# Kernel optimization log

Hardware: AMD Instinct MI355X
Metric: run time of the kernel (lower is better)

Reference implementation:

```python
import jax, jax.numpy as jnp
import numpy as np

N = 100000   # particles
D = 100      # grid cells per dimension


def setup_inputs() -> dict:
    rng = np.random.default_rng(0)
    d = 0.05  # cell_size in source
    # distinct cells (module assumes one particle per cell)
    cells = rng.choice(D ** 3, size=N, replace=False)
    cz = cells // (D * D)
    cy = (cells // D) % D
    cx = cells % D
    jit = rng.uniform(-0.3, 0.3, size=(3, N)) * d  # |jitter| < 0.5*d keeps round(pos/d)==cell
    x = cx * d + jit[0]
    y = cy * d + jit[1]
    z = cz * d + jit[2]
    v = rng.standard_normal((3, N)) * 0.1
    kn = 60000.0
    restitution = 0.5
    alpha = -np.log(restitution) / np.pi
    gamma = alpha / np.sqrt(alpha ** 2 + 1.0)
    rho_p = 2700.0
    particle_mass = 4.0 / 3.0 * 3.1415 * d ** 3 * rho_p
    eta = 2.0 * gamma * np.sqrt(kn * particle_mass / 2.0)
    return {
        "compressed_x_grid": jnp.asarray(x, jnp.float32),
        "compressed_y_grid": jnp.asarray(y, jnp.float32),
        "compressed_z_grid": jnp.asarray(z, jnp.float32),
        "compressed_vx_grid": jnp.asarray(v[0], jnp.float32),
        "compressed_vy_grid": jnp.asarray(v[1], jnp.float32),
        "compressed_vz_grid": jnp.asarray(v[2], jnp.float32),
        "d": float(d),
        "kn": float(kn),
        "damping_coefficient_Eta": float(eta),
        "friction_coefficient": 0.5,
        "dt": 0.001,
        "input_shape": D,
        "filter_size": 5,
    }


def _forces(x, y, z, vx, vy, vz, d, kn, eta, grid_dim, filter_size):
    n = x.shape[0]
    eps = 1e-4
    # cell indices exactly as in the torch code: round(pos/d)
    cx = jnp.round(x / d).astype(jnp.int32)
    cy = jnp.round(y / d).astype(jnp.int32)
    cz = jnp.round(z / d).astype(jnp.int32)
    # dense particle-index grid; -1 = empty (replaces mask + particle_number_tensor)
    idx = -jnp.ones((grid_dim, grid_dim, grid_dim), jnp.int32)
    idx = idx.at[cz, cy, cx].set(jnp.arange(n, dtype=jnp.int32))
    # all filter_size^3 roll offsets; torch.roll wraps, so use modular indexing
    r = filter_size // 2
    ar = jnp.arange(-r, r + 1)
    off = jnp.stack(jnp.meshgrid(ar, ar, ar, indexing="ij"), axis=-1).reshape(-1, 3)  # [K,3] (sz,sy,sx)
    # pair (A at cell c) with (B at cell c - s): mask_contact_A==2 <=> occ[c] & occ[c-s]
    nz = (cz[:, None] - off[None, :, 0]) % grid_dim  # [N,K]
    ny = (cy[:, None] - off[None, :, 1]) % grid_dim
    nx = (cx[:, None] - off[None, :, 2]) % grid_dim
    B = idx[nz, ny, nx]                                   # [N,K] neighbor particle id or -1
    me = jnp.arange(n, dtype=jnp.int32)[:, None]
    valid = (B >= 0) & (B != me)                          # filters empty cells and self pairs (A != B)
    Bs = jnp.where(valid, B, 0)
    dxp = x[:, None] - x[Bs]
    dyp = y[:, None] - y[Bs]
    dzp = z[:, None] - z[Bs]
    dvx = vx[:, None] - vx[Bs]
    dvy = vy[:, None] - vy[Bs]
    dvz = vz[:, None] - vz[Bs]
    dist = jnp.sqrt(dxp * dxp + dyp * dyp + dzp * dzp)
    denom = jnp.maximum(eps, dist)
    contact = valid & (dist < 2.0 * d)
    # spring (collision) force on A, aggregated over neighbors (row-sum == scatter_add to A)
    coef = jnp.where(contact, kn * (dist - 2.0 * d) / denom, 0.0)
    fx_c = (coef * dxp).sum(axis=1)
    fy_c = (coef * dyp).sum(axis=1)
    fz_c = (coef * dzp).sum(axis=1)
    # normal damping force
    vn = (dvx * dxp + dvy * dyp + dvz * dzp) / denom
    dcoef = jnp.where(contact, eta * vn / denom, 0.0)
    fx_d = (dcoef * dxp).sum(axis=1)
    fy_d = (dcoef * dyp).sum(axis=1)
    fz_d = (dcoef * dzp).sum(axis=1)
    return jnp.stack([fx_c, fy_c, fz_c, fx_d, fy_d, fz_d])  # [6, N]


def reference(compressed_x_grid, compressed_y_grid, compressed_z_grid, compressed_vx_grid, compressed_vy_grid, compressed_vz_grid, d, kn, damping_coefficient_Eta, friction_coefficient, dt, input_shape, filter_size):
    return _forces(compressed_x_grid, compressed_y_grid, compressed_z_grid,
                   compressed_vx_grid, compressed_vy_grid, compressed_vz_grid,
                   d, kn, damping_coefficient_Eta, input_shape, filter_size)
```

## Files before the change

### kernel.cpp

```cpp
#include <hip/hip_runtime.h>

static const int DG = 100;
static const int PGD = DG + 4;
static const int PPLANE = PGD * PGD;
static const int PCELLS = PGD * PGD * PGD;


__global__ __launch_bounds__(256) void scatter_kernel(
    const float* __restrict__ x, const float* __restrict__ y, const float* __restrict__ z,
    const float* __restrict__ dptr, int* __restrict__ cell_idx, int n)
{
    int i = blockIdx.x * blockDim.x + threadIdx.x;
    if (i >= n) return;
    float inv_d = 1.0f / dptr[0];
    int cx = (int)roundf(x[i] * inv_d);
    int cy = (int)roundf(y[i] * inv_d);
    int cz = (int)roundf(z[i] * inv_d);
    cell_idx[((cz + 2) * PGD + (cy + 2)) * PGD + (cx + 2)] = i;
}

__global__ __launch_bounds__(256) void force_kernel(
    const float* __restrict__ x, const float* __restrict__ y, const float* __restrict__ z,
    const float* __restrict__ vx, const float* __restrict__ vy, const float* __restrict__ vz,
    const float* __restrict__ dptr, const float* __restrict__ knptr,
    const float* __restrict__ etaptr,
    const int* __restrict__ cell_idx, float* __restrict__ out, int n)
{
    int wid  = blockIdx.x * (blockDim.x >> 6) + (threadIdx.x >> 6);
    if (wid >= n) return;
    int lane = threadIdx.x & 63;
    int p = __builtin_amdgcn_readfirstlane(wid);

    float d    = dptr[0];
    float kn   = knptr[0];
    float eta  = etaptr[0];
    float inv_d = 1.0f / d;
    float two_d = 2.0f * d;

    float px = x[p], py = y[p], pz = z[p];
    float pvx = vx[p], pvy = vy[p], pvz = vz[p];
    int cx = (int)roundf(px * inv_d);
    int cy = (int)roundf(py * inv_d);
    int cz = (int)roundf(pz * inv_d);
    int base = ((cz + 2) * PGD + (cy + 2)) * PGD + (cx + 2);
    base = __builtin_amdgcn_readfirstlane(base);
    const int* __restrict__ g = cell_idx + base;

    int k1 = lane;
    int sz = k1 / 25; int r = k1 - sz * 25; int sy = r / 5; int sx = r - sy * 5;
    int off1 = (sz - 2) * PPLANE + (sy - 2) * PGD + (sx - 2);
    int k2 = lane + 64;
    bool has2 = (k2 < 125);
    int off2 = 0;
    if (has2) {
        sz = k2 / 25; r = k2 - sz * 25; sy = r / 5; sx = r - sy * 5;
        off2 = (sz - 2) * PPLANE + (sy - 2) * PGD + (sx - 2);
    }

    int B1 = g[off1];
    int B2 = has2 ? g[off2] : -1;

    float fxc = 0.f, fyc = 0.f, fzc = 0.f;
    float fxd = 0.f, fyd = 0.f, fzd = 0.f;

    #pragma unroll
    for (int t = 0; t < 2; ++t) {
        int B = (t == 0) ? B1 : B2;
        if (B >= 0 && B != p) {
            float dxp = px - x[B];
            float dyp = py - y[B];
            float dzp = pz - z[B];
            float d2 = dxp * dxp + dyp * dyp + dzp * dzp;
            float dist = __builtin_amdgcn_sqrtf(d2);
            if (dist < two_d) {
                float denom   = fmaxf(1e-4f, dist);
                float inv_den = __builtin_amdgcn_rcpf(denom);
                float coef = kn * (dist - two_d) * inv_den;
                fxc += coef * dxp; fyc += coef * dyp; fzc += coef * dzp;
                float dvxp = pvx - vx[B];
                float dvyp = pvy - vy[B];
                float dvzp = pvz - vz[B];
                float vn    = (dvxp * dxp + dvyp * dyp + dvzp * dzp) * inv_den;
                float dcoef = eta * vn * inv_den;
                fxd += dcoef * dxp; fyd += dcoef * dyp; fzd += dcoef * dzp;
            }
        }
    }

    #pragma unroll
    for (int off = 32; off >= 1; off >>= 1) {
        fxc += __shfl_xor(fxc, off, 64);
        fyc += __shfl_xor(fyc, off, 64);
        fzc += __shfl_xor(fzc, off, 64);
        fxd += __shfl_xor(fxd, off, 64);
        fyd += __shfl_xor(fyd, off, 64);
        fzd += __shfl_xor(fzd, off, 64);
    }

    if (lane < 6) {
        float v = (lane == 0) ? fxc
                : (lane == 1) ? fyc
                : (lane == 2) ? fzc
                : (lane == 3) ? fxd
                : (lane == 4) ? fyd : fzd;
        out[lane * n + p] = v;
    }
}

extern "C" void kernel_launch(void* const* d_in, const int* in_sizes, int n_in,
                              void* d_out, int out_size, void* d_ws, size_t ws_size,
                              hipStream_t stream)
{
    const float* x     = (const float*)d_in[0];
    const float* y     = (const float*)d_in[1];
    const float* z     = (const float*)d_in[2];
    const float* vx    = (const float*)d_in[3];
    const float* vy    = (const float*)d_in[4];
    const float* vz    = (const float*)d_in[5];
    const float* dptr  = (const float*)d_in[6];
    const float* knptr = (const float*)d_in[7];
    const float* etap  = (const float*)d_in[8];
    int n = in_sizes[0];

    int* cell_idx = (int*)d_ws;
    hipMemsetAsync(cell_idx, 0xFF, (size_t)PCELLS * sizeof(int), stream);

    int sblocks = (n + 255) / 256;
    scatter_kernel<<<sblocks, 256, 0, stream>>>(x, y, z, dptr, cell_idx, n);

    const int waves_per_block = 4;
    int fblocks = (n + waves_per_block - 1) / waves_per_block;
    force_kernel<<<fblocks, 256, 0, stream>>>(x, y, z, vx, vy, vz,
                                              dptr, knptr, etap,
                                              cell_idx, (float*)d_out, n);
}
```

Baseline: 136.2 us.

## Store particle positions and ids in cell grid as float4 to remove dependent gathers

The scatter pass now writes each particle's position plus its index as a float4 into the padded cell grid, and packs velocities into a float4 array. The force kernel reads a neighbour's position and id in one load instead of an index load followed by three coordinate gathers, and fetches velocity as one vector load only on contact. Lanes beyond the 125 offsets are redirected to the centre cell so the second load is unconditional. The cost is a four-times-larger grid memset and more workspace.

```diff
diff --git a/kernel.cpp b/kernel.cpp
--- a/kernel.cpp
+++ b/kernel.cpp
@@ -8,23 +8,32 @@
 
 __global__ __launch_bounds__(256) void scatter_kernel(
     const float* __restrict__ x, const float* __restrict__ y, const float* __restrict__ z,
-    const float* __restrict__ dptr, int* __restrict__ cell_idx, int n)
+    const float* __restrict__ vx, const float* __restrict__ vy, const float* __restrict__ vz,
+    const float* __restrict__ dptr,
+    float4* __restrict__ posid, float4* __restrict__ vel4, int n)
 {
     int i = blockIdx.x * blockDim.x + threadIdx.x;
     if (i >= n) return;
     float inv_d = 1.0f / dptr[0];
-    int cx = (int)roundf(x[i] * inv_d);
-    int cy = (int)roundf(y[i] * inv_d);
-    int cz = (int)roundf(z[i] * inv_d);
-    cell_idx[((cz + 2) * PGD + (cy + 2)) * PGD + (cx + 2)] = i;
+    float xi = x[i], yi = y[i], zi = z[i];
+    int cx = (int)roundf(xi * inv_d);
+    int cy = (int)roundf(yi * inv_d);
+    int cz = (int)roundf(zi * inv_d);
+    int cell = ((cz + 2) * PGD + (cy + 2)) * PGD + (cx + 2);
+    float4 pv;
+    pv.x = xi; pv.y = yi; pv.z = zi; pv.w = __int_as_float(i);
+    posid[cell] = pv;
+    float4 vv;
+    vv.x = vx[i]; vv.y = vy[i]; vv.z = vz[i]; vv.w = 0.0f;
+    vel4[i] = vv;
 }
 
 __global__ __launch_bounds__(256) void force_kernel(
     const float* __restrict__ x, const float* __restrict__ y, const float* __restrict__ z,
-    const float* __restrict__ vx, const float* __restrict__ vy, const float* __restrict__ vz,
     const float* __restrict__ dptr, const float* __restrict__ knptr,
     const float* __restrict__ etaptr,
-    const int* __restrict__ cell_idx, float* __restrict__ out, int n)
+    const float4* __restrict__ posid, const float4* __restrict__ vel4,
+    float* __restrict__ out, int n)
 {
     int wid  = blockIdx.x * (blockDim.x >> 6) + (threadIdx.x >> 6);
     if (wid >= n) return;
@@ -38,38 +47,33 @@
     float two_d = 2.0f * d;
 
     float px = x[p], py = y[p], pz = z[p];
-    float pvx = vx[p], pvy = vy[p], pvz = vz[p];
+    float4 pvel = vel4[p];
     int cx = (int)roundf(px * inv_d);
     int cy = (int)roundf(py * inv_d);
     int cz = (int)roundf(pz * inv_d);
     int base = ((cz + 2) * PGD + (cy + 2)) * PGD + (cx + 2);
     base = __builtin_amdgcn_readfirstlane(base);
-    const int* __restrict__ g = cell_idx + base;
+    const float4* __restrict__ g = posid + base;
 
     int k1 = lane;
     int sz = k1 / 25; int r = k1 - sz * 25; int sy = r / 5; int sx = r - sy * 5;
     int off1 = (sz - 2) * PPLANE + (sy - 2) * PGD + (sx - 2);
     int k2 = lane + 64;
-    bool has2 = (k2 < 125);
-    int off2 = 0;
-    if (has2) {
-        sz = k2 / 25; r = k2 - sz * 25; sy = r / 5; sx = r - sy * 5;
-        off2 = (sz - 2) * PPLANE + (sy - 2) * PGD + (sx - 2);
-    }
-
-    int B1 = g[off1];
-    int B2 = has2 ? g[off2] : -1;
+    if (k2 > 124) k2 = 62;
+    sz = k2 / 25; r = k2 - sz * 25; sy = r / 5; sx = r - sy * 5;
+    int off2 = (sz - 2) * PPLANE + (sy - 2) * PGD + (sx - 2);
 
     float fxc = 0.f, fyc = 0.f, fzc = 0.f;
     float fxd = 0.f, fyd = 0.f, fzd = 0.f;
 
     #pragma unroll
     for (int t = 0; t < 2; ++t) {
-        int B = (t == 0) ? B1 : B2;
+        float4 nb = g[t == 0 ? off1 : off2];
+        int B = __float_as_int(nb.w);
         if (B >= 0 && B != p) {
-            float dxp = px - x[B];
-            float dyp = py - y[B];
-            float dzp = pz - z[B];
+            float dxp = px - nb.x;
+            float dyp = py - nb.y;
+            float dzp = pz - nb.z;
             float d2 = dxp * dxp + dyp * dyp + dzp * dzp;
             float dist = __builtin_amdgcn_sqrtf(d2);
             if (dist < two_d) {
@@ -77,9 +81,10 @@
                 float inv_den = __builtin_amdgcn_rcpf(denom);
                 float coef = kn * (dist - two_d) * inv_den;
                 fxc += coef * dxp; fyc += coef * dyp; fzc += coef * dzp;
-                float dvxp = pvx - vx[B];
-                float dvyp = pvy - vy[B];
-                float dvzp = pvz - vz[B];
+                float4 bv = vel4[B];
+                float dvxp = pvel.x - bv.x;
+                float dvyp = pvel.y - bv.y;
+                float dvzp = pvel.z - bv.z;
                 float vn    = (dvxp * dxp + dvyp * dyp + dvzp * dzp) * inv_den;
                 float dcoef = eta * vn * inv_den;
                 fxd += dcoef * dxp; fyd += dcoef * dyp; fzd += dcoef * dzp;
@@ -122,15 +127,17 @@
     const float* etap  = (const float*)d_in[8];
     int n = in_sizes[0];
 
-    int* cell_idx = (int*)d_ws;
-    hipMemsetAsync(cell_idx, 0xFF, (size_t)PCELLS * sizeof(int), stream);
+    float4* posid = (float4*)d_ws;
+    float4* vel4  = (float4*)((char*)d_ws + (size_t)PCELLS * sizeof(float4));
+
+    hipMemsetAsync(posid, 0xFF, (size_t)PCELLS * sizeof(float4), stream);
 
     int sblocks = (n + 255) / 256;
-    scatter_kernel<<<sblocks, 256, 0, stream>>>(x, y, z, dptr, cell_idx, n);
+    scatter_kernel<<<sblocks, 256, 0, stream>>>(x, y, z, vx, vy, vz, dptr,
+                                                posid, vel4, n);
 
     const int waves_per_block = 4;
     int fblocks = (n + waves_per_block - 1) / waves_per_block;
-    force_kernel<<<fblocks, 256, 0, stream>>>(x, y, z, vx, vy, vz,
-                                              dptr, knptr, etap,
-                                              cell_idx, (float*)d_out, n);
+    force_kernel<<<fblocks, 256, 0, stream>>>(x, y, z, dptr, knptr, etap,
+                                              posid, vel4, (float*)d_out, n);
 }
```

New measurement: 153.4 us. 1.13x slower.
